# Kernel tuning notes

Measured on AMD Instinct MI355X. Metric: run time of the kernel, lower is better.

Reference implementation:

```python
import jax, jax.numpy as jnp
import numpy as np

B, N, D, H = 4096, 257, 16, 128  # batch, agents(incl ego), input_dim, hidden_dim


def setup_inputs() -> dict:
    key = jax.random.key(0)
    k1, k2, k3, k4, k5, k6 = jax.random.split(key, 6)
    x = jax.random.normal(k1, (B, N, D), dtype=jnp.float32)
    # columns 6,7,8 are one-hot type flags (vehicle / pedestrian / barrier)
    tidx = jax.random.randint(k2, (B, N), 0, 3)
    onehot = jax.nn.one_hot(tidx, 3, dtype=jnp.float32)
    x = x.at[:, :, 6:9].set(onehot)
    # Linear params (torch convention: y = x @ W.T + b)
    W_fc = jax.random.normal(k3, (H, D), dtype=jnp.float32) / np.sqrt(D)
    b_fc = jax.random.normal(k4, (H,), dtype=jnp.float32) * 0.01
    W_agg = jax.random.normal(k5, (H, H), dtype=jnp.float32) / np.sqrt(H)
    b_agg = jax.random.normal(k6, (H,), dtype=jnp.float32) * 0.01
    return {"agent_tensor": x, "W_fc": W_fc, "b_fc": b_fc,
            "W_agg": W_agg, "b_agg": b_agg}


def reference(agent_tensor, W_fc, b_fc, W_agg, b_agg):
    x = agent_tensor.astype(jnp.float32)
    ego_pos = x[:, 0, :2]            # [B, 2]
    agents = x[:, 1:, :]             # [B, N-1, D]
    # distance-based weights
    dists = jnp.linalg.norm(agents[:, :, :2] - ego_pos[:, None, :], axis=-1)  # [B, N-1]
    w = 1.0 / (dists + 1.0)
    # vehicle flag multiplies weight by 5 (pedestrian/barrier multipliers are 1.0 -> no-op)
    w = jnp.where(agents[:, :, 6] == 1, w * 5.0, w)
    w = w / (jnp.sum(w, axis=-1, keepdims=True) + 1e-10)
    # per-agent embedding + weighted aggregation
    emb = jax.nn.relu(jnp.einsum('bnd,hd->bnh', agents, W_fc) + b_fc)  # [B, N-1, H]
    agg = jnp.einsum('bn,bnh->bh', w, emb)                              # [B, H]
    return jnp.einsum('bh,gh->bg', jax.nn.relu(agg), W_agg) + b_agg    # [B, H]
```

## Files before the change

kernel.cpp:

```cpp
#include <hip/hip_runtime.h>


typedef _Float16 half_t;
typedef half_t f16x8 __attribute__((ext_vector_type(8)));
typedef float f32x4 __attribute__((ext_vector_type(4)));
typedef float f32x16 __attribute__((ext_vector_type(16)));

__global__ __launch_bounds__(256)
__attribute__((amdgpu_waves_per_eu(4, 4)))
void agg_kernel(
    const float* __restrict__ x,
    const float* __restrict__ Wfc,
    const float* __restrict__ bfc,
    float* __restrict__ p_ws,
    float* __restrict__ s_ws)
{
    const int t    = threadIdx.x;
    const int lane = t & 63;
    const int wv   = t >> 6;
    const int W    = blockIdx.x * 4 + wv;
    const int b    = W >> 1;
    const int hf   = W & 1;
    const int lm   = lane & 31;
    const int hi   = lane >> 5;

    __shared__ float wls[4][128];

    const float* xb = x + (size_t)b * (257 * 16);
    const int row0 = 1 + hf * 128;

    float4 a0[4], a1[4];
    #pragma unroll
    for (int tm = 0; tm < 4; ++tm) {
        const float* rp = xb + (size_t)(row0 + tm * 32 + lm) * 16 + hi * 8;
        a0[tm] = *(const float4*)rp;
        a1[tm] = *(const float4*)(rp + 4);
    }

    f16x8 bfr[4];
    #pragma unroll
    for (int ct = 0; ct < 4; ++ct) {
        const float* wp = Wfc + (size_t)(ct * 32 + lm) * 16 + hi * 8;
        const float4 w0 = *(const float4*)wp;
        const float4 w1 = *(const float4*)(wp + 4);
        bfr[ct] = (f16x8){(half_t)w0.x, (half_t)w0.y, (half_t)w0.z, (half_t)w0.w,
                          (half_t)w1.x, (half_t)w1.y, (half_t)w1.z, (half_t)w1.w};
    }

    float nb[4];
    #pragma unroll
    for (int ct = 0; ct < 4; ++ct) nb[ct] = -bfc[ct * 32 + lm];

    const float2 ego = *(const float2*)xb;

    float wsum = 0.f;
    if (hi == 0) {
        #pragma unroll
        for (int tm = 0; tm < 4; ++tm) {
            const float dx = a0[tm].x - ego.x;
            const float dy = a0[tm].y - ego.y;
            float w = 1.0f / (sqrtf(dx * dx + dy * dy) + 1.0f);
            if (a1[tm].z == 1.0f) w *= 5.0f;
            wls[wv][tm * 32 + lm] = w;
            wsum += w;
        }
    }
    #pragma unroll
    for (int off = 32; off > 0; off >>= 1) wsum += __shfl_xor(wsum, off);

    f16x8 afr[4];
    #pragma unroll
    for (int tm = 0; tm < 4; ++tm)
        afr[tm] = (f16x8){(half_t)a0[tm].x, (half_t)a0[tm].y, (half_t)a0[tm].z, (half_t)a0[tm].w,
                          (half_t)a1[tm].x, (half_t)a1[tm].y, (half_t)a1[tm].z, (half_t)a1[tm].w};

    float pacc[4] = {0.f, 0.f, 0.f, 0.f};
    #pragma unroll
    for (int tm = 0; tm < 4; ++tm) {
        float4 w4[4];
        #pragma unroll
        for (int q = 0; q < 4; ++q)
            w4[q] = *(const float4*)(&wls[wv][tm * 32 + q * 8 + hi * 4]);
        #pragma unroll
        for (int ct = 0; ct < 4; ++ct) {
            f32x16 zc = {};
            const f32x16 d = __builtin_amdgcn_mfma_f32_32x32x16_f16(afr[tm], bfr[ct], zc, 0, 0, 0);
            #pragma unroll
            for (int r = 0; r < 16; ++r)
                pacc[ct] = fmaf(w4[r >> 2][r & 3], fmaxf(d[r], nb[ct]), pacc[ct]);
        }
    }

    #pragma unroll
    for (int ct = 0; ct < 4; ++ct) pacc[ct] += __shfl_xor(pacc[ct], 32);
    if (hi == 0) {
        float* pp = p_ws + ((size_t)b * 2 + hf) * 128;
        #pragma unroll
        for (int ct = 0; ct < 4; ++ct) pp[ct * 32 + lm] = pacc[ct];
        if (lane == 0) s_ws[b * 2 + hf] = wsum;
    }
}

__global__ __launch_bounds__(256)
__attribute__((amdgpu_waves_per_eu(4, 4)))
void out_kernel(
    const float* __restrict__ p_ws,
    const float* __restrict__ s_ws,
    const float* __restrict__ bfc,
    const float* __restrict__ Wagg,
    const float* __restrict__ bagg,
    float* __restrict__ out)
{
    const int t    = threadIdx.x;
    const int lane = t & 63;
    const int wv   = t >> 6;
    const int j    = blockIdx.x * 4 + wv;
    const int mt   = j >> 3;
    const int ct   = j & 7;
    const int lr   = lane & 15;
    const int lq   = lane >> 4;

    const int brow = mt * 16 + lr;
    const float2 s2 = *(const float2*)(s_ws + brow * 2);
    const float inv = 1.0f / (s2.x + s2.y + 1e-10f);

    const int col = ct * 16 + lr;
    const float bb = bagg[col];
    f32x4 acc = (f32x4){bb, bb, bb, bb};

    const float* pbase = p_ws + (size_t)brow * 256;
    const float* wrow  = Wagg + (size_t)col * 128;

    #pragma unroll
    for (int kk = 0; kk < 4; ++kk) {
        const int k0 = kk * 32 + lq * 8;
        const float4 p00 = *(const float4*)(pbase + k0);
        const float4 p01 = *(const float4*)(pbase + k0 + 4);
        const float4 p10 = *(const float4*)(pbase + 128 + k0);
        const float4 p11 = *(const float4*)(pbase + 128 + k0 + 4);
        const float4 bf0 = *(const float4*)(bfc + k0);
        const float4 bf1 = *(const float4*)(bfc + k0 + 4);
        const f16x8 afr = (f16x8){
            (half_t)fmaxf(fmaf(p00.x + p10.x, inv, bf0.x), 0.f),
            (half_t)fmaxf(fmaf(p00.y + p10.y, inv, bf0.y), 0.f),
            (half_t)fmaxf(fmaf(p00.z + p10.z, inv, bf0.z), 0.f),
            (half_t)fmaxf(fmaf(p00.w + p10.w, inv, bf0.w), 0.f),
            (half_t)fmaxf(fmaf(p01.x + p11.x, inv, bf1.x), 0.f),
            (half_t)fmaxf(fmaf(p01.y + p11.y, inv, bf1.y), 0.f),
            (half_t)fmaxf(fmaf(p01.z + p11.z, inv, bf1.z), 0.f),
            (half_t)fmaxf(fmaf(p01.w + p11.w, inv, bf1.w), 0.f)};
        const float4 wg0 = *(const float4*)(wrow + k0);
        const float4 wg1 = *(const float4*)(wrow + k0 + 4);
        const f16x8 bfr = (f16x8){(half_t)wg0.x, (half_t)wg0.y, (half_t)wg0.z, (half_t)wg0.w,
                                  (half_t)wg1.x, (half_t)wg1.y, (half_t)wg1.z, (half_t)wg1.w};
        acc = __builtin_amdgcn_mfma_f32_16x16x32_f16(afr, bfr, acc, 0, 0, 0);
    }

    #pragma unroll
    for (int jj = 0; jj < 4; ++jj)
        out[(size_t)(mt * 16 + lq * 4 + jj) * 128 + col] = acc[jj];
}

extern "C" void kernel_launch(void* const* d_in, const int* in_sizes, int n_in,
                              void* d_out, int out_size, void* d_ws, size_t ws_size,
                              hipStream_t stream) {
    const float* x    = (const float*)d_in[0];
    const float* Wfc  = (const float*)d_in[1];
    const float* bfc  = (const float*)d_in[2];
    const float* Wagg = (const float*)d_in[3];
    const float* bagg = (const float*)d_in[4];
    float* out = (float*)d_out;

    float* p_ws = (float*)d_ws;
    float* s_ws = p_ws + (size_t)4096 * 256;

    agg_kernel<<<dim3(2048), dim3(256), 0, stream>>>(x, Wfc, bfc, p_ws, s_ws);
    out_kernel<<<dim3(512), dim3(256), 0, stream>>>(p_ws, s_ws, bfc, Wagg, bagg, out);
}
```

Baseline: 30.99 us.

## Split each batch row across four waves and store partials in fp16

The aggregation kernel now gives each wave 64 agents instead of 128, so each batch row spans four waves and the grid doubles to 4096 blocks. Partial sums go to the workspace as fp16 with four partials per row, and the output kernel sums all four. Occupancy hints are loosened to let more waves fit per EU. The goal is more parallelism and latency hiding for the memory-bound input read. The cost is a second pass that reads the same amount of partial data, repeated W_fc loads per wave, and precision loss from storing unnormalized partial sums in fp16.

```diff
diff --git a/kernel.cpp b/kernel.cpp
--- a/kernel.cpp
+++ b/kernel.cpp
@@ -7,37 +7,38 @@
 typedef float f32x16 __attribute__((ext_vector_type(16)));
 
 __global__ __launch_bounds__(256)
-__attribute__((amdgpu_waves_per_eu(4, 4)))
+__attribute__((amdgpu_waves_per_eu(5, 8)))
 void agg_kernel(
     const float* __restrict__ x,
     const float* __restrict__ Wfc,
     const float* __restrict__ bfc,
-    float* __restrict__ p_ws,
+    half_t* __restrict__ p_ws,
     float* __restrict__ s_ws)
 {
     const int t    = threadIdx.x;
     const int lane = t & 63;
     const int wv   = t >> 6;
     const int W    = blockIdx.x * 4 + wv;
-    const int b    = W >> 1;
-    const int hf   = W & 1;
+    const int b    = W >> 2;
+    const int q    = W & 3;
     const int lm   = lane & 31;
     const int hi   = lane >> 5;
 
-    __shared__ float wls[4][128];
+    __shared__ float wls[4][64];
 
     const float* xb = x + (size_t)b * (257 * 16);
-    const int row0 = 1 + hf * 128;
+    const int row0 = 1 + q * 64;
 
-    float4 a0[4], a1[4];
+    float4 a0[2], a1[2];
     #pragma unroll
-    for (int tm = 0; tm < 4; ++tm) {
+    for (int tm = 0; tm < 2; ++tm) {
         const float* rp = xb + (size_t)(row0 + tm * 32 + lm) * 16 + hi * 8;
         a0[tm] = *(const float4*)rp;
         a1[tm] = *(const float4*)(rp + 4);
     }
 
     f16x8 bfr[4];
+    float nb[4];
     #pragma unroll
     for (int ct = 0; ct < 4; ++ct) {
         const float* wp = Wfc + (size_t)(ct * 32 + lm) * 16 + hi * 8;
@@ -45,18 +46,15 @@
         const float4 w1 = *(const float4*)(wp + 4);
         bfr[ct] = (f16x8){(half_t)w0.x, (half_t)w0.y, (half_t)w0.z, (half_t)w0.w,
                           (half_t)w1.x, (half_t)w1.y, (half_t)w1.z, (half_t)w1.w};
+        nb[ct] = -bfc[ct * 32 + lm];
     }
-
-    float nb[4];
-    #pragma unroll
-    for (int ct = 0; ct < 4; ++ct) nb[ct] = -bfc[ct * 32 + lm];
 
     const float2 ego = *(const float2*)xb;
 
     float wsum = 0.f;
     if (hi == 0) {
         #pragma unroll
-        for (int tm = 0; tm < 4; ++tm) {
+        for (int tm = 0; tm < 2; ++tm) {
             const float dx = a0[tm].x - ego.x;
             const float dy = a0[tm].y - ego.y;
             float w = 1.0f / (sqrtf(dx * dx + dy * dy) + 1.0f);
@@ -68,19 +66,19 @@
     #pragma unroll
     for (int off = 32; off > 0; off >>= 1) wsum += __shfl_xor(wsum, off);
 
-    f16x8 afr[4];
+    f16x8 afr[2];
     #pragma unroll
-    for (int tm = 0; tm < 4; ++tm)
+    for (int tm = 0; tm < 2; ++tm)
         afr[tm] = (f16x8){(half_t)a0[tm].x, (half_t)a0[tm].y, (half_t)a0[tm].z, (half_t)a0[tm].w,
                           (half_t)a1[tm].x, (half_t)a1[tm].y, (half_t)a1[tm].z, (half_t)a1[tm].w};
 
     float pacc[4] = {0.f, 0.f, 0.f, 0.f};
     #pragma unroll
-    for (int tm = 0; tm < 4; ++tm) {
+    for (int tm = 0; tm < 2; ++tm) {
         float4 w4[4];
         #pragma unroll
-        for (int q = 0; q < 4; ++q)
-            w4[q] = *(const float4*)(&wls[wv][tm * 32 + q * 8 + hi * 4]);
+        for (int g = 0; g < 4; ++g)
+            w4[g] = *(const float4*)(&wls[wv][tm * 32 + g * 8 + hi * 4]);
         #pragma unroll
         for (int ct = 0; ct < 4; ++ct) {
             f32x16 zc = {};
@@ -94,17 +92,17 @@
     #pragma unroll
     for (int ct = 0; ct < 4; ++ct) pacc[ct] += __shfl_xor(pacc[ct], 32);
     if (hi == 0) {
-        float* pp = p_ws + ((size_t)b * 2 + hf) * 128;
+        half_t* pp = p_ws + ((size_t)b * 4 + q) * 128;
         #pragma unroll
-        for (int ct = 0; ct < 4; ++ct) pp[ct * 32 + lm] = pacc[ct];
-        if (lane == 0) s_ws[b * 2 + hf] = wsum;
+        for (int ct = 0; ct < 4; ++ct) pp[ct * 32 + lm] = (half_t)pacc[ct];
+        if (lane == 0) s_ws[b * 4 + q] = wsum;
     }
 }
 
 __global__ __launch_bounds__(256)
-__attribute__((amdgpu_waves_per_eu(4, 4)))
+__attribute__((amdgpu_waves_per_eu(4, 8)))
 void out_kernel(
-    const float* __restrict__ p_ws,
+    const half_t* __restrict__ p_ws,
     const float* __restrict__ s_ws,
     const float* __restrict__ bfc,
     const float* __restrict__ Wagg,
@@ -121,34 +119,34 @@
     const int lq   = lane >> 4;
 
     const int brow = mt * 16 + lr;
-    const float2 s2 = *(const float2*)(s_ws + brow * 2);
-    const float inv = 1.0f / (s2.x + s2.y + 1e-10f);
+    const float4 s4 = *(const float4*)(s_ws + brow * 4);
+    const float inv = 1.0f / (s4.x + s4.y + s4.z + s4.w + 1e-10f);
 
     const int col = ct * 16 + lr;
     const float bb = bagg[col];
     f32x4 acc = (f32x4){bb, bb, bb, bb};
 
-    const float* pbase = p_ws + (size_t)brow * 256;
-    const float* wrow  = Wagg + (size_t)col * 128;
+    const half_t* pb  = p_ws + (size_t)brow * 512;
+    const float* wrow = Wagg + (size_t)col * 128;
 
     #pragma unroll
     for (int kk = 0; kk < 4; ++kk) {
         const int k0 = kk * 32 + lq * 8;
-        const float4 p00 = *(const float4*)(pbase + k0);
-        const float4 p01 = *(const float4*)(pbase + k0 + 4);
-        const float4 p10 = *(const float4*)(pbase + 128 + k0);
-        const float4 p11 = *(const float4*)(pbase + 128 + k0 + 4);
+        const f16x8 p0 = *(const f16x8*)(pb + k0);
+        const f16x8 p1 = *(const f16x8*)(pb + 128 + k0);
+        const f16x8 p2 = *(const f16x8*)(pb + 256 + k0);
+        const f16x8 p3 = *(const f16x8*)(pb + 384 + k0);
         const float4 bf0 = *(const float4*)(bfc + k0);
         const float4 bf1 = *(const float4*)(bfc + k0 + 4);
-        const f16x8 afr = (f16x8){
-            (half_t)fmaxf(fmaf(p00.x + p10.x, inv, bf0.x), 0.f),
-            (half_t)fmaxf(fmaf(p00.y + p10.y, inv, bf0.y), 0.f),
-            (half_t)fmaxf(fmaf(p00.z + p10.z, inv, bf0.z), 0.f),
-            (half_t)fmaxf(fmaf(p00.w + p10.w, inv, bf0.w), 0.f),
-            (half_t)fmaxf(fmaf(p01.x + p11.x, inv, bf1.x), 0.f),
-            (half_t)fmaxf(fmaf(p01.y + p11.y, inv, bf1.y), 0.f),
-            (half_t)fmaxf(fmaf(p01.z + p11.z, inv, bf1.z), 0.f),
-            (half_t)fmaxf(fmaf(p01.w + p11.w, inv, bf1.w), 0.f)};
+        float e[8];
+        #pragma unroll
+        for (int i = 0; i < 8; ++i) {
+            const float s = (float)p0[i] + (float)p1[i] + (float)p2[i] + (float)p3[i];
+            const float bv = (i < 4) ? (&bf0.x)[i] : (&bf1.x)[i - 4];
+            e[i] = fmaxf(fmaf(s, inv, bv), 0.f);
+        }
+        const f16x8 afr = (f16x8){(half_t)e[0], (half_t)e[1], (half_t)e[2], (half_t)e[3],
+                                  (half_t)e[4], (half_t)e[5], (half_t)e[6], (half_t)e[7]};
         const float4 wg0 = *(const float4*)(wrow + k0);
         const float4 wg1 = *(const float4*)(wrow + k0 + 4);
         const f16x8 bfr = (f16x8){(half_t)wg0.x, (half_t)wg0.y, (half_t)wg0.z, (half_t)wg0.w,
@@ -171,9 +169,9 @@
     const float* bagg = (const float*)d_in[4];
     float* out = (float*)d_out;
 
-    float* p_ws = (float*)d_ws;
-    float* s_ws = p_ws + (size_t)4096 * 256;
+    half_t* p_ws = (half_t*)d_ws;
+    float*  s_ws = (float*)((char*)d_ws + (size_t)4096 * 512 * sizeof(half_t));
 
-    agg_kernel<<<dim3(2048), dim3(256), 0, stream>>>(x, Wfc, bfc, p_ws, s_ws);
+    agg_kernel<<<dim3(4096), dim3(256), 0, stream>>>(x, Wfc, bfc, p_ws, s_ws);
     out_kernel<<<dim3(512), dim3(256), 0, stream>>>(p_ws, s_ws, bfc, Wagg, bagg, out);
 }
```

Result: slower. 39.30 us (+26.8%).
